# Optimization experiments

Hardware: AMD Instinct MI355X
Metric: run time of the kernel (lower is better)

## Reference

```python
import jax, jax.numpy as jnp
import numpy as np

B, S, D, H = 16, 2048, 128, 4
HD = D // H  # 32
EPS = 1e-5


def layer_norm(x, g, b):
    m = jnp.mean(x, axis=-1, keepdims=True)
    v = jnp.mean((x - m) ** 2, axis=-1, keepdims=True)
    return (x - m) * jax.lax.rsqrt(v + EPS) * g + b


def setup_inputs() -> dict:
    key = jax.random.key(0)
    ks = jax.random.split(key, 9)
    lin = lambda k: jax.random.normal(k, (D, D), dtype=jnp.float32) * 0.01  # [in, out]
    return {
        "input0": jax.random.normal(ks[0], (B, S, D), dtype=jnp.float32),
        "Wq": lin(ks[1]), "bq": jnp.zeros((D,), jnp.float32),
        "Wk": lin(ks[2]), "bk": jnp.zeros((D,), jnp.float32),
        "Wv": lin(ks[3]), "bv": jnp.zeros((D,), jnp.float32),
        "Wo": lin(ks[4]), "bo": jnp.zeros((D,), jnp.float32),
        "g1": jnp.ones((D,), jnp.float32), "b1": jnp.zeros((D,), jnp.float32),
        "W1": lin(ks[5]), "bf1": jnp.zeros((D,), jnp.float32),
        "W2": lin(ks[6]), "bf2": jnp.zeros((D,), jnp.float32),
        "g2": jnp.ones((D,), jnp.float32), "b2": jnp.zeros((D,), jnp.float32),
    }


def reference(input0, Wq, bq, Wk, bk, Wv, bv, Wo, bo, g1, b1, W1, bf1, W2, bf2, g2, b2):
    x = input0
    # multi-head attention (self-attention), dropout in eval mode (identity)
    q = (x @ Wq + bq).reshape(B, S, H, HD)
    k = (x @ Wk + bk).reshape(B, S, H, HD)
    v = (x @ Wv + bv).reshape(B, S, H, HD)
    scores = jnp.einsum("bqhd,bkhd->bhqk", q, k) / jnp.sqrt(jnp.float32(HD))
    weights = jax.nn.softmax(scores, axis=-1)
    attn = jnp.einsum("bhqk,bkhd->bqhd", weights, v).reshape(B, S, D)
    attn = attn @ Wo + bo
    attended = layer_norm(attn + x, g1, b1)
    # feed-forward; note residual uses x (not attended), faithful to source
    ff = jax.nn.relu(attended @ W1 + bf1) @ W2 + bf2
    return layer_norm(ff + x, g2, b2)
```

## Files before the change

kernel.cpp:

```cpp
#include <hip/hip_runtime.h>
#include <math.h>

#define NB   16
#define NS   2048
#define ND   128
#define NH   4
#define NHD  32
#define NROWS (NB * NS)

typedef unsigned short u16;
typedef __bf16 bf16x8 __attribute__((ext_vector_type(8)));
typedef float  f32x4  __attribute__((ext_vector_type(4)));
typedef float  f32x16 __attribute__((ext_vector_type(16)));

static __device__ __forceinline__ u16 f2bf(float a) {
    union { __bf16 h; u16 u; } t; t.h = (__bf16)a; return t.u;
}
static __device__ __forceinline__ unsigned int pk2(float a, float b) {
    union { __bf16 h[2]; unsigned int u; } t;
    t.h[0] = (__bf16)a; t.h[1] = (__bf16)b; return t.u;
}

#if __has_builtin(__builtin_amdgcn_exp2f)
#define EXP2(x) __builtin_amdgcn_exp2f(x)
#else
extern "C" __device__ float __ocml_native_exp2_f32(float);
#define EXP2(x) __ocml_native_exp2_f32(x)
#endif

#define QSCALE (0.17677669529663687f * 1.4426950408889634f)

__global__ __launch_bounds__(256) void prep_kernel(
    const float* __restrict__ Wq, const float* __restrict__ Wk,
    const float* __restrict__ Wv, const float* __restrict__ Wo,
    const float* __restrict__ W1, const float* __restrict__ W2,
    u16* __restrict__ wt)
{
    const int wb = blockIdx.x, tid = threadIdx.x;
    const int widx = wb >> 3, sub = wb & 7;
    const float* W = widx == 0 ? Wq : widx == 1 ? Wk : widx == 2 ? Wv
                   : widx == 3 ? Wo : widx == 4 ? W1 : W2;
    const int flat8 = sub * 256 + tid;
    const int n = flat8 >> 4, k0 = (flat8 & 15) * 8;
    float v[8];
    #pragma unroll
    for (int j = 0; j < 8; ++j) v[j] = W[(size_t)(k0 + j) * ND + n];
    int4 o;
    o.x = pk2(v[0], v[1]); o.y = pk2(v[2], v[3]);
    o.z = pk2(v[4], v[5]); o.w = pk2(v[6], v[7]);
    *reinterpret_cast<int4*>(wt + (size_t)widx * 16384 + (size_t)n * ND + k0) = o;
}

__global__ __launch_bounds__(256) void qkv_mfma_kernel(
    const float* __restrict__ x,
    const u16* __restrict__ wtq, const u16* __restrict__ wtk, const u16* __restrict__ wtv,
    const float* __restrict__ bq, const float* __restrict__ bk, const float* __restrict__ bv,
    u16* __restrict__ qo, u16* __restrict__ kfo, u16* __restrict__ vfo)
{
    __shared__ __align__(16) u16 tileQ[64][136];
    __shared__ __align__(16) u16 tileK[64][136];

    const int tid = threadIdx.x, lane = tid & 63, w = tid >> 6;
    const int n = lane & 15, c = lane >> 4;
    const int row0 = blockIdx.x * 64;
    const int grow = row0 + w * 16;

    bf16x8 a[4];
    #pragma unroll
    for (int kk = 0; kk < 4; ++kk) {
        const float* xp = x + (size_t)(grow + n) * ND + kk * 32 + c * 8;
        float4 f0 = *reinterpret_cast<const float4*>(xp);
        float4 f1 = *reinterpret_cast<const float4*>(xp + 4);
        union { unsigned int u[4]; bf16x8 v; } t;
        t.u[0] = pk2(f0.x, f0.y); t.u[1] = pk2(f0.z, f0.w);
        t.u[2] = pk2(f1.x, f1.y); t.u[3] = pk2(f1.z, f1.w);
        a[kk] = t.v;
    }

    f32x4 accq[8], acck[8], accv[8];
    #pragma unroll
    for (int nb = 0; nb < 8; ++nb) {
        accq[nb] = f32x4{0.f, 0.f, 0.f, 0.f};
        acck[nb] = f32x4{0.f, 0.f, 0.f, 0.f};
        accv[nb] = f32x4{0.f, 0.f, 0.f, 0.f};
    }

    #pragma unroll
    for (int kk = 0; kk < 4; ++kk) {
        #pragma unroll
        for (int nb = 0; nb < 8; ++nb) {
            const size_t boff = (size_t)(nb * 16 + n) * ND + kk * 32 + c * 8;
            bf16x8 bqf = *reinterpret_cast<const bf16x8*>(wtq + boff);
            bf16x8 bkf = *reinterpret_cast<const bf16x8*>(wtk + boff);
            bf16x8 bvf = *reinterpret_cast<const bf16x8*>(wtv + boff);
            accq[nb] = __builtin_amdgcn_mfma_f32_16x16x32_bf16(a[kk], bqf, accq[nb], 0, 0, 0);
            acck[nb] = __builtin_amdgcn_mfma_f32_16x16x32_bf16(a[kk], bkf, acck[nb], 0, 0, 0);
            accv[nb] = __builtin_amdgcn_mfma_f32_16x16x32_bf16(a[kk], bvf, accv[nb], 0, 0, 0);
        }
    }

    const int b    = row0 >> 11;
    const int sp0b = row0 & (NS - 1);
    const int sp0  = sp0b + w * 16;

    #pragma unroll
    for (int nb = 0; nb < 8; ++nb) {
        const int col = nb * 16 + n, hh = col >> 5, d32 = col & 31;
        const float bqv = bq[col], bkv = bk[col], bvv = bv[col];
        const size_t kvb = ((size_t)b * NH + hh) * (NS * NHD);

        #pragma unroll
        for (int r = 0; r < 4; ++r) {
            tileQ[w * 16 + 4 * c + r][col] = f2bf((accq[nb][r] + bqv) * QSCALE);
            tileK[w * 16 + 4 * c + r][col] = f2bf(acck[nb][r] + bkv);
        }

        const int lanep = d32 + 32 * (c & 1);
        const int j0    = 4 * (c >> 1);
        float v0 = accv[nb][0] + bvv, v1 = accv[nb][1] + bvv;
        float v2 = accv[nb][2] + bvv, v3 = accv[nb][3] + bvv;
        *reinterpret_cast<uint2*>(
            vfo + kvb + (size_t)(sp0 >> 4) * 512 + (size_t)lanep * 8 + j0) =
            make_uint2(pk2(v0, v1), pk2(v2, v3));
    }

    {
        const int lk = w * 16 + (lane >> 2);
        const int gk = sp0b + lk;
        const int T = gk >> 5, l5 = gk & 31;
        #pragma unroll
        for (int i = 0; i < 4; ++i) {
            const int m16  = (lane & 3) + 4 * i;
            const int col0 = m16 * 8;
            const int hh = col0 >> 5, d32 = col0 & 31;
            const int s = d32 >> 4, c2 = (d32 >> 3) & 1;
            const size_t kvb = ((size_t)b * NH + hh) * (NS * NHD);
            int4 qv = *reinterpret_cast<const int4*>(&tileQ[lk][col0]);
            *reinterpret_cast<int4*>(qo + kvb + (size_t)gk * NHD + d32) = qv;
            int4 kv = *reinterpret_cast<const int4*>(&tileK[lk][col0]);
            *reinterpret_cast<int4*>(
                kfo + kvb + (size_t)(T * 2 + s) * 512 + (size_t)(l5 + 32 * c2) * 8) = kv;
        }
    }
}

__global__ __launch_bounds__(256) void attn_mfma_kernel(
    const u16* __restrict__ qg,
    const u16* __restrict__ kfg,
    const u16* __restrict__ vfg,
    u16* __restrict__ ao)
{
    __shared__ float Ol[3][64][17];
    __shared__ float Dl[3][64];

    const int tid = threadIdx.x, lane = tid & 63, w = tid >> 6;

    const int bid  = blockIdx.x;
    const int bh   = (bid & 7) * 8 + ((bid >> 3) & 7);
    const int qblk = bid >> 6;
    const int b = bh >> 2, h = bh & 3;
    const int n = lane & 31, hf = lane >> 5;
    const size_t fbase = (size_t)bh * (NS * NHD);
    const int q0w = qblk * 32;

    const bf16x8 qf0 = *reinterpret_cast<const bf16x8*>(
        qg + fbase + (size_t)(q0w + n) * NHD + 8 * hf);
    const bf16x8 qf1 = *reinterpret_cast<const bf16x8*>(
        qg + fbase + (size_t)(q0w + n) * NHD + 16 + 8 * hf);

    union { unsigned int u[4]; bf16x8 v; } ONES;
    ONES.u[0] = 0x3F803F80u; ONES.u[1] = 0x3F803F80u;
    ONES.u[2] = 0x3F803F80u; ONES.u[3] = 0x3F803F80u;

    f32x16 ot, dn, zz;
    #pragma unroll
    for (int i = 0; i < 16; ++i) { ot[i] = 0.f; dn[i] = 0.f; zz[i] = 0.f; }

    const u16* kf = kfg + fbase + (size_t)lane * 8 + (size_t)w * 16384;
    const u16* vf = vfg + fbase + (size_t)lane * 8 + (size_t)w * 16384;

    auto EXPPACK = [&](const f32x16& s, bf16x8& w0, bf16x8& w1) {
        union { unsigned int u[4]; bf16x8 v; } a0, a1;
        #pragma unroll
        for (int i = 0; i < 4; ++i)
            a0.u[i] = pk2(EXP2(s[2 * i]), EXP2(s[2 * i + 1]));
        #pragma unroll
        for (int i = 0; i < 4; ++i)
            a1.u[i] = pk2(EXP2(s[8 + 2 * i]), EXP2(s[9 + 2 * i]));
        w0 = a0.v; w1 = a1.v;
    };

    bf16x8 ka0 = *reinterpret_cast<const bf16x8*>(kf);
    bf16x8 ka1 = *reinterpret_cast<const bf16x8*>(kf + 512);
    bf16x8 va0 = *reinterpret_cast<const bf16x8*>(vf);
    bf16x8 va1 = *reinterpret_cast<const bf16x8*>(vf + 512);

    for (int t = 0; t < 16; ++t) {
        kf += 1024; vf += 1024;

        __builtin_amdgcn_s_setprio(1);
        f32x16 s = __builtin_amdgcn_mfma_f32_32x32x16_bf16(ka0, qf0, zz, 0, 0, 0);
        s = __builtin_amdgcn_mfma_f32_32x32x16_bf16(ka1, qf1, s, 0, 0, 0);
        __builtin_amdgcn_s_setprio(0);

        bf16x8 nka0 = *reinterpret_cast<const bf16x8*>(kf);
        bf16x8 nka1 = *reinterpret_cast<const bf16x8*>(kf + 512);

        bf16x8 pw0, pw1;
        EXPPACK(s, pw0, pw1);

        __builtin_amdgcn_s_setprio(1);
        ot = __builtin_amdgcn_mfma_f32_32x32x16_bf16(va0, pw0, ot, 0, 0, 0);
        dn = __builtin_amdgcn_mfma_f32_32x32x16_bf16(ONES.v, pw0, dn, 0, 0, 0);
        ot = __builtin_amdgcn_mfma_f32_32x32x16_bf16(va1, pw1, ot, 0, 0, 0);
        dn = __builtin_amdgcn_mfma_f32_32x32x16_bf16(ONES.v, pw1, dn, 0, 0, 0);
        __builtin_amdgcn_s_setprio(0);

        va0 = *reinterpret_cast<const bf16x8*>(vf);
        va1 = *reinterpret_cast<const bf16x8*>(vf + 512);
        ka0 = nka0; ka1 = nka1;
    }

    if (w > 0) {
        #pragma unroll
        for (int i = 0; i < 16; ++i) Ol[w - 1][lane][i] = ot[i];
        Dl[w - 1][lane] = dn[0];
    }
    __syncthreads();
    if (w == 0) {
        #pragma unroll
        for (int j = 0; j < 3; ++j)
            #pragma unroll
            for (int i = 0; i < 16; ++i) ot[i] += Ol[j][lane][i];
        const float dnt = dn[0] + Dl[0][lane] + Dl[1][lane] + Dl[2][lane];
        const float inv = 1.0f / dnt;

        u16* orow = ao + ((size_t)b * NS + q0w + n) * ND + h * NHD + 4 * hf;
        #pragma unroll
        for (int g = 0; g < 4; ++g) {
            uint2 wv = make_uint2(pk2(ot[4 * g] * inv, ot[4 * g + 1] * inv),
                                  pk2(ot[4 * g + 2] * inv, ot[4 * g + 3] * inv));
            *reinterpret_cast<uint2*>(orow + 8 * g) = wv;
        }
    }
}

__global__ __launch_bounds__(256) void tail_kernel(
    const u16* __restrict__ A0, const u16* __restrict__ wto,
    const u16* __restrict__ wt1, const u16* __restrict__ wt2,
    const float* __restrict__ bo, const float* __restrict__ bf1,
    const float* __restrict__ bf2, const float* __restrict__ x,
    const float* __restrict__ g1, const float* __restrict__ b1,
    const float* __restrict__ g2, const float* __restrict__ b2,
    float* __restrict__ outp)
{
    __shared__ __align__(16) u16 tile[64][136];
    const int tid = threadIdx.x, lane = tid & 63, w = tid >> 6;
    const int n = lane & 15, c = lane >> 4;
    const int row0 = blockIdx.x * 64;
    const int grow = row0 + w * 16;
    const int lrow = w * 16;

    bf16x8 a[4];
    f32x4 acc[8];

    float xres[8][4];
    #pragma unroll
    for (int nb = 0; nb < 8; ++nb) {
        const int col = nb * 16 + n;
        #pragma unroll
        for (int r = 0; r < 4; ++r)
            xres[nb][r] = x[(size_t)(grow + 4 * c + r) * ND + col];
    }

    #pragma unroll
    for (int kk = 0; kk < 4; ++kk)
        a[kk] = *reinterpret_cast<const bf16x8*>(
            A0 + (size_t)(grow + n) * ND + kk * 32 + c * 8);
    #pragma unroll
    for (int nb = 0; nb < 8; ++nb) acc[nb] = f32x4{0.f, 0.f, 0.f, 0.f};
    #pragma unroll
    for (int kk = 0; kk < 4; ++kk)
        #pragma unroll
        for (int nb = 0; nb < 8; ++nb) {
            bf16x8 bw = *reinterpret_cast<const bf16x8*>(
                wto + (size_t)(nb * 16 + n) * ND + kk * 32 + c * 8);
            acc[nb] = __builtin_amdgcn_mfma_f32_16x16x32_bf16(a[kk], bw, acc[nb], 0, 0, 0);
        }

    {
        float vals[8][4];
        float sr[4]  = {0.f, 0.f, 0.f, 0.f};
        float sr2[4] = {0.f, 0.f, 0.f, 0.f};
        #pragma unroll
        for (int nb = 0; nb < 8; ++nb) {
            const int col = nb * 16 + n;
            const float bb = bo[col];
            #pragma unroll
            for (int r = 0; r < 4; ++r) {
                float vv = acc[nb][r] + bb + xres[nb][r];
                vals[nb][r] = vv;
                sr[r]  += vv;
                sr2[r] += vv * vv;
            }
        }
        #pragma unroll
        for (int m = 1; m < 16; m <<= 1)
            #pragma unroll
            for (int r = 0; r < 4; ++r) {
                sr[r]  += __shfl_xor(sr[r],  m);
                sr2[r] += __shfl_xor(sr2[r], m);
            }
        #pragma unroll
        for (int r = 0; r < 4; ++r) {
            float mean = sr[r] * (1.f / 128.f);
            float var  = fmaf(-mean, mean, sr2[r] * (1.f / 128.f));
            float rstd = rsqrtf(var + 1e-5f);
            #pragma unroll
            for (int nb = 0; nb < 8; ++nb) {
                const int col = nb * 16 + n;
                float y = fmaf((vals[nb][r] - mean) * rstd, g1[col], b1[col]);
                tile[lrow + 4 * c + r][col] = f2bf(y);
            }
        }
    }
    __syncthreads();

    #pragma unroll
    for (int kk = 0; kk < 4; ++kk)
        a[kk] = *reinterpret_cast<const bf16x8*>(&tile[lrow + n][kk * 32 + c * 8]);
    __syncthreads();
    #pragma unroll
    for (int nb = 0; nb < 8; ++nb) acc[nb] = f32x4{0.f, 0.f, 0.f, 0.f};
    #pragma unroll
    for (int kk = 0; kk < 4; ++kk)
        #pragma unroll
        for (int nb = 0; nb < 8; ++nb) {
            bf16x8 bw = *reinterpret_cast<const bf16x8*>(
                wt1 + (size_t)(nb * 16 + n) * ND + kk * 32 + c * 8);
            acc[nb] = __builtin_amdgcn_mfma_f32_16x16x32_bf16(a[kk], bw, acc[nb], 0, 0, 0);
        }
    #pragma unroll
    for (int nb = 0; nb < 8; ++nb) {
        const int col = nb * 16 + n;
        const float bb = bf1[col];
        #pragma unroll
        for (int r = 0; r < 4; ++r)
            tile[lrow + 4 * c + r][col] = f2bf(fmaxf(acc[nb][r] + bb, 0.f));
    }
    __syncthreads();

    #pragma unroll
    for (int kk = 0; kk < 4; ++kk)
        a[kk] = *reinterpret_cast<const bf16x8*>(&tile[lrow + n][kk * 32 + c * 8]);
    #pragma unroll
    for (int nb = 0; nb < 8; ++nb) acc[nb] = f32x4{0.f, 0.f, 0.f, 0.f};
    #pragma unroll
    for (int kk = 0; kk < 4; ++kk)
        #pragma unroll
        for (int nb = 0; nb < 8; ++nb) {
            bf16x8 bw = *reinterpret_cast<const bf16x8*>(
                wt2 + (size_t)(nb * 16 + n) * ND + kk * 32 + c * 8);
            acc[nb] = __builtin_amdgcn_mfma_f32_16x16x32_bf16(a[kk], bw, acc[nb], 0, 0, 0);
        }
    {
        float vals[8][4];
        float sr[4]  = {0.f, 0.f, 0.f, 0.f};
        float sr2[4] = {0.f, 0.f, 0.f, 0.f};
        #pragma unroll
        for (int nb = 0; nb < 8; ++nb) {
            const int col = nb * 16 + n;
            const float bb = bf2[col];
            #pragma unroll
            for (int r = 0; r < 4; ++r) {
                float vv = acc[nb][r] + bb + xres[nb][r];
                vals[nb][r] = vv;
                sr[r]  += vv;
                sr2[r] += vv * vv;
            }
        }
        #pragma unroll
        for (int m = 1; m < 16; m <<= 1)
            #pragma unroll
            for (int r = 0; r < 4; ++r) {
                sr[r]  += __shfl_xor(sr[r],  m);
                sr2[r] += __shfl_xor(sr2[r], m);
            }
        #pragma unroll
        for (int r = 0; r < 4; ++r) {
            float mean = sr[r] * (1.f / 128.f);
            float var  = fmaf(-mean, mean, sr2[r] * (1.f / 128.f));
            float rstd = rsqrtf(var + 1e-5f);
            #pragma unroll
            for (int nb = 0; nb < 8; ++nb) {
                const int col = nb * 16 + n;
                float y = fmaf((vals[nb][r] - mean) * rstd, g2[col], b2[col]);
                outp[(size_t)(grow + 4 * c + r) * ND + col] = y;
            }
        }
    }
}

extern "C" void kernel_launch(void* const* d_in, const int* in_sizes, int n_in,
                              void* d_out, int out_size, void* d_ws, size_t ws_size,
                              hipStream_t stream)
{
    const float* x   = (const float*)d_in[0];
    const float* Wq  = (const float*)d_in[1];
    const float* bq  = (const float*)d_in[2];
    const float* Wk  = (const float*)d_in[3];
    const float* bk  = (const float*)d_in[4];
    const float* Wv  = (const float*)d_in[5];
    const float* bv  = (const float*)d_in[6];
    const float* Wo  = (const float*)d_in[7];
    const float* bo  = (const float*)d_in[8];
    const float* g1  = (const float*)d_in[9];
    const float* b1  = (const float*)d_in[10];
    const float* W1  = (const float*)d_in[11];
    const float* bf1 = (const float*)d_in[12];
    const float* W2  = (const float*)d_in[13];
    const float* bf2 = (const float*)d_in[14];
    const float* g2  = (const float*)d_in[15];
    const float* b2  = (const float*)d_in[16];
    float* outp = (float*)d_out;

    const size_t NE = (size_t)NROWS * ND;
    u16* wt  = (u16*)d_ws;
    u16* qb  = wt + 6 * 16384;
    u16* kfb = qb + NE;
    u16* vfb = kfb + NE;
    u16* aob = vfb + NE;

    dim3 blk(256);
    prep_kernel<<<dim3(48), blk, 0, stream>>>(Wq, Wk, Wv, Wo, W1, W2, wt);
    qkv_mfma_kernel<<<dim3(NROWS / 64), blk, 0, stream>>>(
        x, wt + 0 * 16384, wt + 1 * 16384, wt + 2 * 16384, bq, bk, bv, qb, kfb, vfb);
    attn_mfma_kernel<<<dim3(4096), blk, 0, stream>>>(qb, kfb, vfb, aob);
    tail_kernel<<<dim3(NROWS / 64), blk, 0, stream>>>(
        aob, wt + 3 * 16384, wt + 4 * 16384, wt + 5 * 16384,
        bo, bf1, bf2, x, g1, b1, g2, b2, outp);
}
```

Measured before the change: 134.7 us.

## Restructure attention to single-wave blocks with interleaved KV layout and split tiles

```diff
diff --git a/kernel.cpp b/kernel.cpp
--- a/kernel.cpp
+++ b/kernel.cpp
@@ -55,15 +55,16 @@
     const float* __restrict__ x,
     const u16* __restrict__ wtq, const u16* __restrict__ wtk, const u16* __restrict__ wtv,
     const float* __restrict__ bq, const float* __restrict__ bk, const float* __restrict__ bv,
-    u16* __restrict__ qo, u16* __restrict__ kfo, u16* __restrict__ vfo)
+    u16* __restrict__ qo, u16* __restrict__ kvf)
 {
-    __shared__ __align__(16) u16 tileQ[64][136];
-    __shared__ __align__(16) u16 tileK[64][136];
+    __shared__ __align__(16) u16 tileQ[32][136];
+    __shared__ __align__(16) u16 tileK[32][136];
 
     const int tid = threadIdx.x, lane = tid & 63, w = tid >> 6;
+    const int rw = w >> 1, cw = w & 1;
     const int n = lane & 15, c = lane >> 4;
-    const int row0 = blockIdx.x * 64;
-    const int grow = row0 + w * 16;
+    const int row0 = blockIdx.x * 32;
+    const int grow = row0 + rw * 16;
 
     bf16x8 a[4];
     #pragma unroll
@@ -77,9 +78,9 @@
         a[kk] = t.v;
     }
 
-    f32x4 accq[8], acck[8], accv[8];
-    #pragma unroll
-    for (int nb = 0; nb < 8; ++nb) {
+    f32x4 accq[4], acck[4], accv[4];
+    #pragma unroll
+    for (int nb = 0; nb < 4; ++nb) {
         accq[nb] = f32x4{0.f, 0.f, 0.f, 0.f};
         acck[nb] = f32x4{0.f, 0.f, 0.f, 0.f};
         accv[nb] = f32x4{0.f, 0.f, 0.f, 0.f};
@@ -88,8 +89,8 @@
     #pragma unroll
     for (int kk = 0; kk < 4; ++kk) {
         #pragma unroll
-        for (int nb = 0; nb < 8; ++nb) {
-            const size_t boff = (size_t)(nb * 16 + n) * ND + kk * 32 + c * 8;
+        for (int nb = 0; nb < 4; ++nb) {
+            const size_t boff = (size_t)(cw * 64 + nb * 16 + n) * ND + kk * 32 + c * 8;
             bf16x8 bqf = *reinterpret_cast<const bf16x8*>(wtq + boff);
             bf16x8 bkf = *reinterpret_cast<const bf16x8*>(wtk + boff);
             bf16x8 bvf = *reinterpret_cast<const bf16x8*>(wtv + boff);
@@ -101,147 +102,135 @@
 
     const int b    = row0 >> 11;
     const int sp0b = row0 & (NS - 1);
-    const int sp0  = sp0b + w * 16;
-
-    #pragma unroll
-    for (int nb = 0; nb < 8; ++nb) {
-        const int col = nb * 16 + n, hh = col >> 5, d32 = col & 31;
+    const int sp0  = sp0b + rw * 16;
+
+    #pragma unroll
+    for (int nb = 0; nb < 4; ++nb) {
+        const int col = cw * 64 + nb * 16 + n, hh = col >> 5, d32 = col & 31;
         const float bqv = bq[col], bkv = bk[col], bvv = bv[col];
-        const size_t kvb = ((size_t)b * NH + hh) * (NS * NHD);
 
         #pragma unroll
         for (int r = 0; r < 4; ++r) {
-            tileQ[w * 16 + 4 * c + r][col] = f2bf((accq[nb][r] + bqv) * QSCALE);
-            tileK[w * 16 + 4 * c + r][col] = f2bf(acck[nb][r] + bkv);
-        }
-
+            tileQ[rw * 16 + 4 * c + r][col] = f2bf((accq[nb][r] + bqv) * QSCALE);
+            tileK[rw * 16 + 4 * c + r][col] = f2bf(acck[nb][r] + bkv);
+        }
+
+        const size_t kvb2 = ((size_t)b * NH + hh) * (2 * NS * NHD);
+        const int u2    = sp0 >> 4;
         const int lanep = d32 + 32 * (c & 1);
         const int j0    = 4 * (c >> 1);
         float v0 = accv[nb][0] + bvv, v1 = accv[nb][1] + bvv;
         float v2 = accv[nb][2] + bvv, v3 = accv[nb][3] + bvv;
         *reinterpret_cast<uint2*>(
-            vfo + kvb + (size_t)(sp0 >> 4) * 512 + (size_t)lanep * 8 + j0) =
+            kvf + kvb2 + (size_t)(u2 >> 1) * 2048 + 1024 + (u2 & 1) * 512
+                + (size_t)lanep * 8 + j0) =
             make_uint2(pk2(v0, v1), pk2(v2, v3));
     }
 
-    {
-        const int lk = w * 16 + (lane >> 2);
+    __syncthreads();
+
+    #pragma unroll
+    for (int i = 0; i < 2; ++i) {
+        const int flat = tid + i * 256;
+        const int lk = flat >> 4, m16 = flat & 15;
+        const int col0 = m16 * 8;
+        const int hh = col0 >> 5, d32 = col0 & 31;
+        const int s2 = d32 >> 4, c22 = (d32 >> 3) & 1;
         const int gk = sp0b + lk;
         const int T = gk >> 5, l5 = gk & 31;
-        #pragma unroll
-        for (int i = 0; i < 4; ++i) {
-            const int m16  = (lane & 3) + 4 * i;
-            const int col0 = m16 * 8;
-            const int hh = col0 >> 5, d32 = col0 & 31;
-            const int s = d32 >> 4, c2 = (d32 >> 3) & 1;
-            const size_t kvb = ((size_t)b * NH + hh) * (NS * NHD);
-            int4 qv = *reinterpret_cast<const int4*>(&tileQ[lk][col0]);
-            *reinterpret_cast<int4*>(qo + kvb + (size_t)gk * NHD + d32) = qv;
-            int4 kv = *reinterpret_cast<const int4*>(&tileK[lk][col0]);
-            *reinterpret_cast<int4*>(
-                kfo + kvb + (size_t)(T * 2 + s) * 512 + (size_t)(l5 + 32 * c2) * 8) = kv;
-        }
-    }
-}
-
-__global__ __launch_bounds__(256) void attn_mfma_kernel(
+        const size_t kvb  = ((size_t)b * NH + hh) * (NS * NHD);
+        const size_t kvb2 = ((size_t)b * NH + hh) * (2 * NS * NHD);
+        int4 qv = *reinterpret_cast<const int4*>(&tileQ[lk][col0]);
+        *reinterpret_cast<int4*>(qo + kvb + (size_t)gk * NHD + d32) = qv;
+        int4 kv = *reinterpret_cast<const int4*>(&tileK[lk][col0]);
+        *reinterpret_cast<int4*>(
+            kvf + kvb2 + (size_t)T * 2048 + s2 * 512 + (size_t)(l5 + 32 * c22) * 8) = kv;
+    }
+}
+
+__global__ __launch_bounds__(64) void attn_mfma_kernel(
     const u16* __restrict__ qg,
-    const u16* __restrict__ kfg,
-    const u16* __restrict__ vfg,
+    const u16* __restrict__ kvf,
     u16* __restrict__ ao)
 {
-    __shared__ float Ol[3][64][17];
-    __shared__ float Dl[3][64];
-
-    const int tid = threadIdx.x, lane = tid & 63, w = tid >> 6;
+    const int lane = threadIdx.x;
 
     const int bid  = blockIdx.x;
     const int bh   = (bid & 7) * 8 + ((bid >> 3) & 7);
     const int qblk = bid >> 6;
     const int b = bh >> 2, h = bh & 3;
     const int n = lane & 31, hf = lane >> 5;
-    const size_t fbase = (size_t)bh * (NS * NHD);
     const int q0w = qblk * 32;
 
+    const size_t qbase = (size_t)bh * (NS * NHD);
     const bf16x8 qf0 = *reinterpret_cast<const bf16x8*>(
-        qg + fbase + (size_t)(q0w + n) * NHD + 8 * hf);
+        qg + qbase + (size_t)(q0w + n) * NHD + 8 * hf);
     const bf16x8 qf1 = *reinterpret_cast<const bf16x8*>(
-        qg + fbase + (size_t)(q0w + n) * NHD + 16 + 8 * hf);
-
-    union { unsigned int u[4]; bf16x8 v; } ONES;
-    ONES.u[0] = 0x3F803F80u; ONES.u[1] = 0x3F803F80u;
-    ONES.u[2] = 0x3F803F80u; ONES.u[3] = 0x3F803F80u;
-
-    f32x16 ot, dn, zz;
-    #pragma unroll
-    for (int i = 0; i < 16; ++i) { ot[i] = 0.f; dn[i] = 0.f; zz[i] = 0.f; }
-
-    const u16* kf = kfg + fbase + (size_t)lane * 8 + (size_t)w * 16384;
-    const u16* vf = vfg + fbase + (size_t)lane * 8 + (size_t)w * 16384;
+        qg + qbase + (size_t)(q0w + n) * NHD + 16 + 8 * hf);
+
+    f32x16 ot, zz;
+    #pragma unroll
+    for (int i = 0; i < 16; ++i) { ot[i] = 0.f; zz[i] = 0.f; }
+    float lp0 = 0.f, lp1 = 0.f;
+
+    const u16* kv = kvf + (size_t)bh * (2 * NS * NHD) + (size_t)lane * 8;
 
     auto EXPPACK = [&](const f32x16& s, bf16x8& w0, bf16x8& w1) {
         union { unsigned int u[4]; bf16x8 v; } a0, a1;
         #pragma unroll
-        for (int i = 0; i < 4; ++i)
-            a0.u[i] = pk2(EXP2(s[2 * i]), EXP2(s[2 * i + 1]));
-        #pragma unroll
-        for (int i = 0; i < 4; ++i)
-            a1.u[i] = pk2(EXP2(s[8 + 2 * i]), EXP2(s[9 + 2 * i]));
+        for (int i = 0; i < 4; ++i) {
+            float p0 = EXP2(s[2 * i]), p1 = EXP2(s[2 * i + 1]);
+            lp0 += p0; lp1 += p1;
+            a0.u[i] = pk2(p0, p1);
+        }
+        #pragma unroll
+        for (int i = 0; i < 4; ++i) {
+            float p0 = EXP2(s[8 + 2 * i]), p1 = EXP2(s[9 + 2 * i]);
+            lp0 += p0; lp1 += p1;
+            a1.u[i] = pk2(p0, p1);
+        }
         w0 = a0.v; w1 = a1.v;
     };
 
-    bf16x8 ka0 = *reinterpret_cast<const bf16x8*>(kf);
-    bf16x8 ka1 = *reinterpret_cast<const bf16x8*>(kf + 512);
-    bf16x8 va0 = *reinterpret_cast<const bf16x8*>(vf);
-    bf16x8 va1 = *reinterpret_cast<const bf16x8*>(vf + 512);
-
-    for (int t = 0; t < 16; ++t) {
-        kf += 1024; vf += 1024;
+    bf16x8 ka0 = *reinterpret_cast<const bf16x8*>(kv);
+    bf16x8 ka1 = *reinterpret_cast<const bf16x8*>(kv + 512);
+    bf16x8 va0 = *reinterpret_cast<const bf16x8*>(kv + 1024);
+    bf16x8 va1 = *reinterpret_cast<const bf16x8*>(kv + 1536);
+
+    for (int t = 0; t < 64; ++t) {
+        kv += 2048;
 
         __builtin_amdgcn_s_setprio(1);
         f32x16 s = __builtin_amdgcn_mfma_f32_32x32x16_bf16(ka0, qf0, zz, 0, 0, 0);
         s = __builtin_amdgcn_mfma_f32_32x32x16_bf16(ka1, qf1, s, 0, 0, 0);
         __builtin_amdgcn_s_setprio(0);
 
-        bf16x8 nka0 = *reinterpret_cast<const bf16x8*>(kf);
-        bf16x8 nka1 = *reinterpret_cast<const bf16x8*>(kf + 512);
+        bf16x8 nka0 = *reinterpret_cast<const bf16x8*>(kv);
+        bf16x8 nka1 = *reinterpret_cast<const bf16x8*>(kv + 512);
 
         bf16x8 pw0, pw1;
         EXPPACK(s, pw0, pw1);
 
         __builtin_amdgcn_s_setprio(1);
         ot = __builtin_amdgcn_mfma_f32_32x32x16_bf16(va0, pw0, ot, 0, 0, 0);
-        dn = __builtin_amdgcn_mfma_f32_32x32x16_bf16(ONES.v, pw0, dn, 0, 0, 0);
         ot = __builtin_amdgcn_mfma_f32_32x32x16_bf16(va1, pw1, ot, 0, 0, 0);
-        dn = __builtin_amdgcn_mfma_f32_32x32x16_bf16(ONES.v, pw1, dn, 0, 0, 0);
         __builtin_amdgcn_s_setprio(0);
 
-        va0 = *reinterpret_cast<const bf16x8*>(vf);
-        va1 = *reinterpret_cast<const bf16x8*>(vf + 512);
+        va0 = *reinterpret_cast<const bf16x8*>(kv + 1024);
+        va1 = *reinterpret_cast<const bf16x8*>(kv + 1536);
         ka0 = nka0; ka1 = nka1;
     }
 
-    if (w > 0) {
-        #pragma unroll
-        for (int i = 0; i < 16; ++i) Ol[w - 1][lane][i] = ot[i];
-        Dl[w - 1][lane] = dn[0];
-    }
-    __syncthreads();
-    if (w == 0) {
-        #pragma unroll
-        for (int j = 0; j < 3; ++j)
-            #pragma unroll
-            for (int i = 0; i < 16; ++i) ot[i] += Ol[j][lane][i];
-        const float dnt = dn[0] + Dl[0][lane] + Dl[1][lane] + Dl[2][lane];
-        const float inv = 1.0f / dnt;
-
-        u16* orow = ao + ((size_t)b * NS + q0w + n) * ND + h * NHD + 4 * hf;
-        #pragma unroll
-        for (int g = 0; g < 4; ++g) {
-            uint2 wv = make_uint2(pk2(ot[4 * g] * inv, ot[4 * g + 1] * inv),
-                                  pk2(ot[4 * g + 2] * inv, ot[4 * g + 3] * inv));
-            *reinterpret_cast<uint2*>(orow + 8 * g) = wv;
-        }
+    float lp  = lp0 + lp1;
+    const float dn  = lp + __shfl_xor(lp, 32);
+    const float inv = 1.0f / dn;
+
+    u16* orow = ao + ((size_t)b * NS + q0w + n) * ND + h * NHD + 4 * hf;
+    #pragma unroll
+    for (int g = 0; g < 4; ++g) {
+        uint2 wv = make_uint2(pk2(ot[4 * g] * inv, ot[4 * g + 1] * inv),
+                              pk2(ot[4 * g + 2] * inv, ot[4 * g + 3] * inv));
+        *reinterpret_cast<uint2*>(orow + 8 * g) = wv;
     }
 }
 
@@ -254,20 +243,24 @@
     const float* __restrict__ g2, const float* __restrict__ b2,
     float* __restrict__ outp)
 {
-    __shared__ __align__(16) u16 tile[64][136];
+    __shared__ __align__(16) u16 tile[32][136];
+    __shared__ float Sl[2][2][16];
+    __shared__ float Sq[2][2][16];
+
     const int tid = threadIdx.x, lane = tid & 63, w = tid >> 6;
+    const int rw = w >> 1, cw = w & 1;
     const int n = lane & 15, c = lane >> 4;
-    const int row0 = blockIdx.x * 64;
-    const int grow = row0 + w * 16;
-    const int lrow = w * 16;
+    const int row0 = blockIdx.x * 32;
+    const int grow = row0 + rw * 16;
+    const int lrow = rw * 16;
 
     bf16x8 a[4];
-    f32x4 acc[8];
-
-    float xres[8][4];
-    #pragma unroll
-    for (int nb = 0; nb < 8; ++nb) {
-        const int col = nb * 16 + n;
+    f32x4 acc[4];
+
+    float xres[4][4];
+    #pragma unroll
+    for (int nb = 0; nb < 4; ++nb) {
+        const int col = cw * 64 + nb * 16 + n;
         #pragma unroll
         for (int r = 0; r < 4; ++r)
             xres[nb][r] = x[(size_t)(grow + 4 * c + r) * ND + col];
@@ -278,24 +271,23 @@
         a[kk] = *reinterpret_cast<const bf16x8*>(
             A0 + (size_t)(grow + n) * ND + kk * 32 + c * 8);
     #pragma unroll
-    for (int nb = 0; nb < 8; ++nb) acc[nb] = f32x4{0.f, 0.f, 0.f, 0.f};
-    #pragma unroll
-    for (int kk = 0; kk < 4; ++kk)
-        #pragma unroll
-        for (int nb = 0; nb < 8; ++nb) {
+    for (int nb = 0; nb < 4; ++nb) acc[nb] = f32x4{0.f, 0.f, 0.f, 0.f};
+    #pragma unroll
+    for (int kk = 0; kk < 4; ++kk)
+        #pragma unroll
+        for (int nb = 0; nb < 4; ++nb) {
             bf16x8 bw = *reinterpret_cast<const bf16x8*>(
-                wto + (size_t)(nb * 16 + n) * ND + kk * 32 + c * 8);
+                wto + (size_t)(cw * 64 + nb * 16 + n) * ND + kk * 32 + c * 8);
             acc[nb] = __builtin_amdgcn_mfma_f32_16x16x32_bf16(a[kk], bw, acc[nb], 0, 0, 0);
         }
 
     {
-        float vals[8][4];
+        float vals[4][4];
         float sr[4]  = {0.f, 0.f, 0.f, 0.f};
         float sr2[4] = {0.f, 0.f, 0.f, 0.f};
         #pragma unroll
-        for (int nb = 0; nb < 8; ++nb) {
-            const int col = nb * 16 + n;
-            const float bb = bo[col];
+        for (int nb = 0; nb < 4; ++nb) {
+            const float bb = bo[cw * 64 + nb * 16 + n];
             #pragma unroll
             for (int r = 0; r < 4; ++r) {
                 float vv = acc[nb][r] + bb + xres[nb][r];
@@ -311,14 +303,24 @@
                 sr[r]  += __shfl_xor(sr[r],  m);
                 sr2[r] += __shfl_xor(sr2[r], m);
             }
+        if (n == 0) {
+            #pragma unroll
+            for (int r = 0; r < 4; ++r) {
+                Sl[rw][cw][4 * c + r] = sr[r];
+                Sq[rw][cw][4 * c + r] = sr2[r];
+            }
+        }
+        __syncthreads();
         #pragma unroll
         for (int r = 0; r < 4; ++r) {
-            float mean = sr[r] * (1.f / 128.f);
-            float var  = fmaf(-mean, mean, sr2[r] * (1.f / 128.f));
+            float st  = Sl[rw][0][4 * c + r] + Sl[rw][1][4 * c + r];
+            float st2 = Sq[rw][0][4 * c + r] + Sq[rw][1][4 * c + r];
+            float mean = st * (1.f / 128.f);
+            float var  = fmaf(-mean, mean, st2 * (1.f / 128.f));
             float rstd = rsqrtf(var + 1e-5f);
             #pragma unroll
-            for (int nb = 0; nb < 8; ++nb) {
-                const int col = nb * 16 + n;
+            for (int nb = 0; nb < 4; ++nb) {
+                const int col = cw * 64 + nb * 16 + n;
                 float y = fmaf((vals[nb][r] - mean) * rstd, g1[col], b1[col]);
                 tile[lrow + 4 * c + r][col] = f2bf(y);
             }
@@ -331,18 +333,18 @@
         a[kk] = *reinterpret_cast<const bf16x8*>(&tile[lrow + n][kk * 32 + c * 8]);
     __syncthreads();
     #pragma unroll
-    for (int nb = 0; nb < 8; ++nb) acc[nb] = f32x4{0.f, 0.f, 0.f, 0.f};
-    #pragma unroll
-    for (int kk = 0; kk < 4; ++kk)
-        #pragma unroll
-        for (int nb = 0; nb < 8; ++nb) {
+    for (int nb = 0; nb < 4; ++nb) acc[nb] = f32x4{0.f, 0.f, 0.f, 0.f};
+    #pragma unroll
+    for (int kk = 0; kk < 4; ++kk)
+        #pragma unroll
+        for (int nb = 0; nb < 4; ++nb) {
             bf16x8 bw = *reinterpret_cast<const bf16x8*>(
-                wt1 + (size_t)(nb * 16 + n) * ND + kk * 32 + c * 8);
+                wt1 + (size_t)(cw * 64 + nb * 16 + n) * ND + kk * 32 + c * 8);
             acc[nb] = __builtin_amdgcn_mfma_f32_16x16x32_bf16(a[kk], bw, acc[nb], 0, 0, 0);
         }
     #pragma unroll
-    for (int nb = 0; nb < 8; ++nb) {
-        const int col = nb * 16 + n;
+    for (int nb = 0; nb < 4; ++nb) {
+        const int col = cw * 64 + nb * 16 + n;
         const float bb = bf1[col];
         #pragma unroll
         for (int r = 0; r < 4; ++r)
@@ -354,23 +356,22 @@
     for (int kk = 0; kk < 4; ++kk)
         a[kk] = *reinterpret_cast<const bf16x8*>(&tile[lrow + n][kk * 32 + c * 8]);
     #pragma unroll
-    for (int nb = 0; nb < 8; ++nb) acc[nb] = f32x4{0.f, 0.f, 0.f, 0.f};
-    #pragma unroll
-    for (int kk = 0; kk < 4; ++kk)
-        #pragma unroll
-        for (int nb = 0; nb < 8; ++nb) {
+    for (int nb = 0; nb < 4; ++nb) acc[nb] = f32x4{0.f, 0.f, 0.f, 0.f};
+    #pragma unroll
+    for (int kk = 0; kk < 4; ++kk)
+        #pragma unroll
+        for (int nb = 0; nb < 4; ++nb) {
             bf16x8 bw = *reinterpret_cast<const bf16x8*>(
-                wt2 + (size_t)(nb * 16 + n) * ND + kk * 32 + c * 8);
+                wt2 + (size_t)(cw * 64 + nb * 16 + n) * ND + kk * 32 + c * 8);
             acc[nb] = __builtin_amdgcn_mfma_f32_16x16x32_bf16(a[kk], bw, acc[nb], 0, 0, 0);
         }
     {
-        float vals[8][4];
+        float vals[4][4];
         float sr[4]  = {0.f, 0.f, 0.f, 0.f};
         float sr2[4] = {0.f, 0.f, 0.f, 0.f};
         #pragma unroll
-        for (int nb = 0; nb < 8; ++nb) {
-            const int col = nb * 16 + n;
-            const float bb = bf2[col];
+        for (int nb = 0; nb < 4; ++nb) {
+            const float bb = bf2[cw * 64 + nb * 16 + n];
             #pragma unroll
             for (int r = 0; r < 4; ++r) {
                 float vv = acc[nb][r] + bb + xres[nb][r];
@@ -386,14 +387,25 @@
                 sr[r]  += __shfl_xor(sr[r],  m);
                 sr2[r] += __shfl_xor(sr2[r], m);
             }
+        __syncthreads();
+        if (n == 0) {
+            #pragma unroll
+            for (int r = 0; r < 4; ++r) {
+                Sl[rw][cw][4 * c + r] = sr[r];
+                Sq[rw][cw][4 * c + r] = sr2[r];
+            }
+        }
+        __syncthreads();
         #pragma unroll
         for (int r = 0; r < 4; ++r) {
-            float mean = sr[r] * (1.f / 128.f);
-            float var  = fmaf(-mean, mean, sr2[r] * (1.f / 128.f));
+            float st  = Sl[rw][0][4 * c + r] + Sl[rw][1][4 * c + r];
+            float st2 = Sq[rw][0][4 * c + r] + Sq[rw][1][4 * c + r];
+            float mean = st * (1.f / 128.f);
+            float var  = fmaf(-mean, mean, st2 * (1.f / 128.f));
             float rstd = rsqrtf(var + 1e-5f);
             #pragma unroll
-            for (int nb = 0; nb < 8; ++nb) {
-                const int col = nb * 16 + n;
+            for (int nb = 0; nb < 4; ++nb) {
+                const int col = cw * 64 + nb * 16 + n;
                 float y = fmaf((vals[nb][r] - mean) * rstd, g2[col], b2[col]);
                 outp[(size_t)(grow + 4 * c + r) * ND + col] = y;
             }
@@ -427,16 +439,14 @@
     const size_t NE = (size_t)NROWS * ND;
     u16* wt  = (u16*)d_ws;
     u16* qb  = wt + 6 * 16384;
-    u16* kfb = qb + NE;
-    u16* vfb = kfb + NE;
-    u16* aob = vfb + NE;
-
-    dim3 blk(256);
-    prep_kernel<<<dim3(48), blk, 0, stream>>>(Wq, Wk, Wv, Wo, W1, W2, wt);
-    qkv_mfma_kernel<<<dim3(NROWS / 64), blk, 0, stream>>>(
-        x, wt + 0 * 16384, wt + 1 * 16384, wt + 2 * 16384, bq, bk, bv, qb, kfb, vfb);
-    attn_mfma_kernel<<<dim3(4096), blk, 0, stream>>>(qb, kfb, vfb, aob);
-    tail_kernel<<<dim3(NROWS / 64), blk, 0, stream>>>(
+    u16* kvb = qb + NE;
+    u16* aob = kvb + 2 * NE;
+
+    prep_kernel<<<dim3(48), dim3(256), 0, stream>>>(Wq, Wk, Wv, Wo, W1, W2, wt);
+    qkv_mfma_kernel<<<dim3(NROWS / 32), dim3(256), 0, stream>>>(
+        x, wt + 0 * 16384, wt + 1 * 16384, wt + 2 * 16384, bq, bk, bv, qb, kvb);
+    attn_mfma_kernel<<<dim3(4096), dim3(64), 0, stream>>>(qb, kvb, aob);
+    tail_kernel<<<dim3(NROWS / 32), dim3(256), 0, stream>>>(
         aob, wt + 3 * 16384, wt + 4 * 16384, wt + 5 * 16384,
         bo, bf1, bf2, x, g1, b1, g2, b2, outp);
 }
```

Measured after the change: 135.7 us. Within noise of the previous version (+0.7%).
